# Kernel tuning notes

Measured on AMD Instinct MI355X. Metric: run time of the kernel, lower is better.

## Reference

```python
import jax, jax.numpy as jnp
import numpy as np

IMAGE = 224; P = 16; G = 14; N = 196; C = 3; PD = 768
DIM = 512; DEPTH = 4; H = 8; DH = 64; INNER = 512; MLP = 2048
SCALE = DIM ** -0.5
EPS = 1e-5


def layernorm(x, g, b):
    m = x.mean(-1, keepdims=True)
    v = ((x - m) ** 2).mean(-1, keepdims=True)
    return (x - m) * jax.lax.rsqrt(v + EPS) * g + b


def compute_embedding(W, coords):
    # W: (DIM//2, 2), coords: (b, p, 2) -> (b, p, DIM)
    proj = jnp.einsum('od,bpd->bpo', W, coords)
    s = (2.0 / (DIM // 2)) ** 0.5
    return jnp.concatenate([s * jnp.cos(proj), s * jnp.sin(proj)], axis=-1)


def setup_inputs():
    key = jax.random.key(0)
    ks = jax.random.split(key, 8)
    B = 64
    img = jax.random.normal(ks[0], (B, C, IMAGE, IMAGE), jnp.float32)
    noise_token = jax.random.normal(ks[1], (B, DIM), jnp.float32)
    A_noise = jax.random.normal(ks[2], (B, 2, 2), jnp.float32)
    b_noise = jax.random.normal(ks[3], (B, 2), jnp.float32)
    m, n = np.meshgrid(np.arange(G), np.arange(G))
    X = jnp.asarray(np.reshape(np.stack((m, n), -1), (-1, 2)), jnp.float32)  # (N,2)
    Wfreq = jax.random.normal(ks[4], (DIM // 2, 2), jnp.float32)  # band_width=1.0
    base_pos = compute_embedding(Wfreq, X[None])  # (1,N,DIM), trainable param
    A_mean = jnp.eye(2, dtype=jnp.float32)
    b_mean = jnp.zeros((2,), jnp.float32)
    A_std = jnp.zeros((2, 2), jnp.float32)  # variance_init = 0.0
    b_std = jnp.zeros((2,), jnp.float32)

    def lin(k, i, o):
        return jax.random.normal(k, (i, o), jnp.float32) / np.float32(np.sqrt(i))

    Wpe = lin(ks[5], PD, DIM); bpe = jnp.zeros((DIM,), jnp.float32)
    Wep = lin(ks[6], DIM, PD); bep = jnp.zeros((PD,), jnp.float32)
    kk = jax.random.split(ks[7], DEPTH * 4)
    Wqkv = jnp.stack([lin(kk[4 * i + 0], DIM, 3 * INNER) for i in range(DEPTH)])
    Wout = jnp.stack([lin(kk[4 * i + 1], INNER, DIM) for i in range(DEPTH)])
    bout = jnp.zeros((DEPTH, DIM), jnp.float32)
    Wff1 = jnp.stack([lin(kk[4 * i + 2], DIM, MLP) for i in range(DEPTH)])
    bff1 = jnp.zeros((DEPTH, MLP), jnp.float32)
    Wff2 = jnp.stack([lin(kk[4 * i + 3], MLP, DIM) for i in range(DEPTH)])
    bff2 = jnp.zeros((DEPTH, DIM), jnp.float32)
    ln1_g = jnp.ones((DEPTH, DIM), jnp.float32); ln1_b = jnp.zeros((DEPTH, DIM), jnp.float32)
    ln2_g = jnp.ones((DEPTH, DIM), jnp.float32); ln2_b = jnp.zeros((DEPTH, DIM), jnp.float32)
    return dict(img=img, noise_token=noise_token, A_noise=A_noise, b_noise=b_noise,
                Wfreq=Wfreq, X=X, base_pos=base_pos,
                A_mean=A_mean, b_mean=b_mean, A_std=A_std, b_std=b_std,
                Wpe=Wpe, bpe=bpe, Wep=Wep, bep=bep,
                ln1_g=ln1_g, ln1_b=ln1_b, Wqkv=Wqkv, Wout=Wout, bout=bout,
                ln2_g=ln2_g, ln2_b=ln2_b, Wff1=Wff1, bff1=bff1, Wff2=Wff2, bff2=bff2)


def reference(img, noise_token, A_noise, b_noise, Wfreq, X, base_pos,
              A_mean, b_mean, A_std, b_std, Wpe, bpe, Wep, bep,
              ln1_g, ln1_b, Wqkv, Wout, bout, ln2_g, ln2_b, Wff1, bff1, Wff2, bff2):
    del noise_token  # deleted in original forward
    B = img.shape[0]
    # patchify: b c (h p1) (w p2) -> b (h w) (p1 p2 c)
    x = img.reshape(B, C, G, P, G, P).transpose(0, 2, 4, 3, 5, 1).reshape(B, N, PD)
    x = x @ Wpe + bpe  # patch_to_embedding
    # transformed positional embedding (_compute_transformed_embedding)
    A = A_mean + jax.nn.softplus(A_std) * A_noise          # (B,2,2)
    bvec = b_mean + jax.nn.softplus(b_std) * b_noise       # (B,2)
    X_t = jnp.einsum('pd,bdo->bpo', X, A) + bvec[:, None, :]
    pos = compute_embedding(Wfreq, X_t)                    # (B,N,DIM)
    # pos-only attention scores: identical across layers and heads
    dots = jnp.einsum('bid,jd->bij', pos, base_pos[0]) * SCALE
    attn = jax.nn.softmax(dots, axis=-1)                   # (B,N,N)
    for l in range(DEPTH):
        # PreNorm(SplitAttention) -- note: NO residual around attention
        xn = layernorm(x, ln1_g[l], ln1_b[l])
        qkv = xn @ Wqkv[l]
        v = qkv[..., 2 * INNER:].reshape(B, N, H, DH).transpose(0, 2, 1, 3)  # b h n d
        out = jnp.einsum('bij,bhjd->bhid', attn, v)
        out = out.transpose(0, 2, 1, 3).reshape(B, N, INNER)
        x = out @ Wout[l] + bout[l]
        # Residual(PreNorm(FeedForward))
        xn2 = layernorm(x, ln2_g[l], ln2_b[l])
        ff = jax.nn.gelu(xn2 @ Wff1[l] + bff1[l], approximate=False) @ Wff2[l] + bff2[l]
        x = ff + x
    x = x @ Wep + bep  # embedding_to_patch
    # unpatchify: b (h w) (p1 p2 c) -> b c (h p1) (w p2)
    return x.reshape(B, G, G, P, P, C).transpose(0, 5, 1, 3, 2, 4).reshape(B, C, IMAGE, IMAGE)
```

## Files before the change

### kernel.cpp

```cpp
#include <hip/hip_runtime.h>
#include <hip/hip_bf16.h>
#include <math.h>


#define B_    64
#define NTOK  196
#define CCH   3
#define PDIM  768
#define DIM   512
#define MLP   2048
#define MROWS (B_ * NTOK)
#define IMGHW 224
#define KPAD  224
#define VTLD  (B_ * KPAD)

typedef __attribute__((ext_vector_type(8))) short bf16x8;
typedef __attribute__((ext_vector_type(4))) float f32x4;

static __device__ __forceinline__ unsigned short f2b(float f) {
    unsigned int x = __float_as_uint(f);
    unsigned int r = (x + 0x7FFFu + ((x >> 16) & 1u)) >> 16;
    return (unsigned short)r;
}
static __device__ __forceinline__ float softplusf(float x) {
    return fmaxf(x, 0.0f) + log1pf(expf(-fabsf(x)));
}

typedef const __attribute__((address_space(1))) unsigned int* gp1_t;
typedef __attribute__((address_space(3))) unsigned int* lp3_t;
static __device__ __forceinline__ void gld16(const unsigned short* g, unsigned short* l) {
    __builtin_amdgcn_global_load_lds((gp1_t)g, (lp3_t)l, 16, 0, 0);
}

__global__ __launch_bounds__(256) void patchify_kernel(const float* __restrict__ img,
                                                       unsigned short* __restrict__ xp) {
    long idx = (long)blockIdx.x * blockDim.x + threadIdx.x;
    if (idx >= (long)MROWS * PDIM) return;
    int pd = (int)(idx % PDIM);
    long bn = idx / PDIM;
    int n = (int)(bn % NTOK);
    int b = (int)(bn / NTOK);
    int c = pd % 3;
    int p12 = pd / 3;
    int p1 = p12 >> 4, p2 = p12 & 15;
    int g1 = n / 14, g2 = n % 14;
    long src = (((long)b * CCH + c) * IMGHW + (g1 * 16 + p1)) * IMGHW + (g2 * 16 + p2);
    xp[idx] = f2b(img[src]);
}

__global__ __launch_bounds__(256) void unpatchify_kernel(const float* __restrict__ y,
                                                         float* __restrict__ out) {
    long idx = (long)blockIdx.x * blockDim.x + threadIdx.x;
    if (idx >= (long)B_ * CCH * IMGHW * IMGHW) return;
    int ww = (int)(idx % IMGHW);
    long r = idx / IMGHW;
    int hh = (int)(r % IMGHW);
    r /= IMGHW;
    int c = (int)(r % CCH);
    int b = (int)(r / CCH);
    int g1 = hh >> 4, p1 = hh & 15;
    int g2 = ww >> 4, p2 = ww & 15;
    int n = g1 * 14 + g2;
    int pd = (p1 * 16 + p2) * 3 + c;
    out[idx] = y[((long)b * NTOK + n) * PDIM + pd];
}

__global__ __launch_bounds__(256) void pos_kernel(const float* __restrict__ Xc,
                                                  const float* __restrict__ Wfreq,
                                                  const float* __restrict__ A_noise,
                                                  const float* __restrict__ b_noise,
                                                  const float* __restrict__ A_mean,
                                                  const float* __restrict__ b_mean,
                                                  const float* __restrict__ A_std,
                                                  const float* __restrict__ b_std,
                                                  unsigned short* __restrict__ pos) {
    int bp = blockIdx.x;
    int b = bp / NTOK, p = bp % NTOK;
    int o = threadIdx.x;
    float a00 = A_mean[0] + softplusf(A_std[0]) * A_noise[b * 4 + 0];
    float a01 = A_mean[1] + softplusf(A_std[1]) * A_noise[b * 4 + 1];
    float a10 = A_mean[2] + softplusf(A_std[2]) * A_noise[b * 4 + 2];
    float a11 = A_mean[3] + softplusf(A_std[3]) * A_noise[b * 4 + 3];
    float bv0 = b_mean[0] + softplusf(b_std[0]) * b_noise[b * 2 + 0];
    float bv1 = b_mean[1] + softplusf(b_std[1]) * b_noise[b * 2 + 1];
    float x0 = Xc[p * 2 + 0], x1 = Xc[p * 2 + 1];
    float xt0 = x0 * a00 + x1 * a10 + bv0;
    float xt1 = x0 * a01 + x1 * a11 + bv1;
    float proj = Wfreq[o * 2 + 0] * xt0 + Wfreq[o * 2 + 1] * xt1;
    float sv, cv;
    sincosf(proj, &sv, &cv);
    const float s = 0.08838834764831843f;
    pos[(long)bp * DIM + o]       = f2b(s * cv);
    pos[(long)bp * DIM + 256 + o] = f2b(s * sv);
}

__global__ __launch_bounds__(64) void softmax_kernel(const float* __restrict__ dots,
                                                     unsigned short* __restrict__ attn) {
    long row = blockIdx.x;
    const float* p = dots + row * NTOK;
    unsigned short* q = attn + row * KPAD;
    int t = threadIdx.x;
    float v[4];
    float mx = -INFINITY;
    #pragma unroll
    for (int j = 0; j < 4; j++) {
        int i = t + j * 64;
        v[j] = (i < NTOK) ? p[i] : -INFINITY;
        mx = fmaxf(mx, v[j]);
    }
    #pragma unroll
    for (int off = 32; off >= 1; off >>= 1) mx = fmaxf(mx, __shfl_xor(mx, off));
    float sum = 0.f;
    #pragma unroll
    for (int j = 0; j < 4; j++) {
        int i = t + j * 64;
        v[j] = (i < NTOK) ? expf(v[j] - mx) : 0.f;
        sum += v[j];
    }
    #pragma unroll
    for (int off = 32; off >= 1; off >>= 1) sum += __shfl_xor(sum, off);
    float inv = 1.0f / sum;
    #pragma unroll
    for (int j = 0; j < 4; j++) {
        int i = t + j * 64;
        if (i < NTOK) q[i] = f2b(v[j] * inv);
        else if (i < KPAD) q[i] = 0;
    }
}

__global__ __launch_bounds__(128) void ln_kernel(const float* __restrict__ x,
                                                 const float* __restrict__ g,
                                                 const float* __restrict__ bb,
                                                 unsigned short* __restrict__ out) {
    long row = blockIdx.x;
    int t = threadIdx.x;
    float4 v = *(const float4*)(x + row * DIM + t * 4);
    float s = v.x + v.y + v.z + v.w;
    float q = v.x * v.x + v.y * v.y + v.z * v.z + v.w * v.w;
    #pragma unroll
    for (int off = 32; off >= 1; off >>= 1) {
        s += __shfl_xor(s, off);
        q += __shfl_xor(q, off);
    }
    __shared__ float red[4];
    int lane = t & 63, wv = t >> 6;
    if (lane == 0) { red[wv * 2] = s; red[wv * 2 + 1] = q; }
    __syncthreads();
    float S = red[0] + red[2], Q = red[1] + red[3];
    float mean = S * (1.0f / DIM);
    float var = Q * (1.0f / DIM) - mean * mean;
    float rs = rsqrtf(var + 1e-5f);
    float4 gg = *(const float4*)(g + t * 4);
    float4 bv = *(const float4*)(bb + t * 4);
    ushort4 o;
    o.x = f2b((v.x - mean) * rs * gg.x + bv.x);
    o.y = f2b((v.y - mean) * rs * gg.y + bv.y);
    o.z = f2b((v.z - mean) * rs * gg.z + bv.z);
    o.w = f2b((v.w - mean) * rs * gg.w + bv.w);
    *(ushort4*)(out + row * DIM + t * 4) = o;
}

struct TDesc {
    const float* in;
    unsigned short* out;
    int R, C, ld, cb, bbase, tx, trans;
};
struct TPack { TDesc d[19]; int n; };

__global__ __launch_bounds__(256) void wconv_kernel(TPack p) {
    __shared__ float t[32][33];
    int bid = blockIdx.x;
    int di = 0;
    for (int i = 1; i < p.n; ++i) if (bid >= p.d[i].bbase) di = i;
    TDesc d = p.d[di];
    int local = bid - d.bbase;
    int bx = local % d.tx, by = local / d.tx;
    int r0 = by * 32, c0 = bx * 32;
    int lx = threadIdx.x & 31, ly = threadIdx.x >> 5;
    if (d.trans) {
        #pragma unroll
        for (int i = 0; i < 4; i++) {
            int r = r0 + ly + i * 8, c = c0 + lx;
            t[ly + i * 8][lx] = (r < d.R && c < d.C) ? d.in[(long)r * d.ld + d.cb + c] : 0.f;
        }
        __syncthreads();
        #pragma unroll
        for (int i = 0; i < 4; i++) {
            int c = c0 + ly + i * 8, r = r0 + lx;
            if (c < d.C && r < d.R) d.out[(long)c * d.R + r] = f2b(t[lx][ly + i * 8]);
        }
    } else {
        #pragma unroll
        for (int i = 0; i < 4; i++) {
            int r = r0 + ly + i * 8, c = c0 + lx;
            if (r < d.R && c < d.C) d.out[(long)r * d.C + c] = f2b(d.in[(long)r * d.ld + d.cb + c]);
        }
    }
}

template <bool GELU, bool RESID, bool WF32, bool WB16>
__global__ __launch_bounds__(256) void mgemm(const unsigned short* __restrict__ A,
                                             const unsigned short* __restrict__ Bt,
                                             const float* __restrict__ bias,
                                             const float* __restrict__ Rsd,
                                             float* __restrict__ Cf,
                                             unsigned short* __restrict__ Cb,
                                             int M, int N, int K,
                                             int lda, int ldb, int ldc,
                                             long bsA, long bsBt, long bsC,
                                             float scale, int grp, int gstride) {
    int bz = blockIdx.z;
    A  += bz * bsA;
    Bt += bz * bsBt;
    __shared__ __attribute__((aligned(1024))) unsigned short As[4096];
    __shared__ __attribute__((aligned(1024))) unsigned short Bs[4096];
    int m0 = blockIdx.y * 128, n0 = blockIdx.x * 128;
    int tid = threadIdx.x;
    int wave = tid >> 6, lane = tid & 63;
    int wm = (wave & 1) * 64, wn = (wave >> 1) * 64;
    int fr = lane & 15, fg = lane >> 4;

    int g1 = wave * 64 + lane;
    int g2 = g1 + 256;
    int f1 = g1 >> 7, r1 = g1 & 127;
    int f2 = g2 >> 7, r2 = g2 & 127;
    int ra1 = m0 + r1; if (ra1 > M - 1) ra1 = M - 1;
    int ra2 = m0 + r2; if (ra2 > M - 1) ra2 = M - 1;
    int rb1 = n0 + r1; if (rb1 > N - 1) rb1 = N - 1;
    int rb2 = n0 + r2; if (rb2 > N - 1) rb2 = N - 1;
    const unsigned short* pa1 = A + (long)ra1 * lda + f1 * 8;
    const unsigned short* pa2 = A + (long)ra2 * lda + f2 * 8;
    const unsigned short* pb1 = Bt + (long)rb1 * ldb + f1 * 8;
    const unsigned short* pb2 = Bt + (long)rb2 * ldb + f2 * 8;
    unsigned short* lA1 = &As[wave * 512];
    unsigned short* lA2 = &As[wave * 512 + 2048];
    unsigned short* lB1 = &Bs[wave * 512];
    unsigned short* lB2 = &Bs[wave * 512 + 2048];

    f32x4 acc[4][4];
    #pragma unroll
    for (int i = 0; i < 4; i++)
        #pragma unroll
        for (int j = 0; j < 4; j++) acc[i][j] = (f32x4)0.f;

    for (int k0 = 0; k0 < K; k0 += 32) {
        __syncthreads();
        gld16(pa1 + k0, lA1);
        gld16(pa2 + k0, lA2);
        gld16(pb1 + k0, lB1);
        gld16(pb2 + k0, lB2);
        __syncthreads();
        bf16x8 af[4], bfr[4];
        #pragma unroll
        for (int i = 0; i < 4; i++)
            af[i]  = *(const bf16x8*)&As[(fg * 128 + wm + i * 16 + fr) * 8];
        #pragma unroll
        for (int j = 0; j < 4; j++)
            bfr[j] = *(const bf16x8*)&Bs[(fg * 128 + wn + j * 16 + fr) * 8];
        #pragma unroll
        for (int i = 0; i < 4; i++)
            #pragma unroll
            for (int j = 0; j < 4; j++)
                acc[i][j] = __builtin_amdgcn_mfma_f32_16x16x32_bf16(af[i], bfr[j], acc[i][j], 0, 0, 0);
    }

    long cbase = (long)bz * bsC;
    #pragma unroll
    for (int i = 0; i < 4; i++) {
        int row = m0 + wm + i * 16 + fg * 4;
        #pragma unroll
        for (int j = 0; j < 4; j++) {
            int col = n0 + wn + j * 16 + fr;
            if (col >= N) continue;
            int ocol = (grp > 0) ? ((col / grp) * gstride + (col % grp)) : col;
            float bv = bias ? bias[col] : 0.f;
            #pragma unroll
            for (int r = 0; r < 4; r++) {
                if (row + r >= M) continue;
                float v = acc[i][j][r] * scale + bv;
                if (GELU) v = 0.5f * v * (1.0f + erff(v * 0.70710678118654752f));
                long ci = cbase + (long)(row + r) * ldc + ocol;
                if (RESID) v += Rsd[ci];
                if (WF32) Cf[ci] = v;
                if (WB16) Cb[ci] = f2b(v);
            }
        }
    }
}


extern "C" void kernel_launch(void* const* d_in, const int* in_sizes, int n_in,
                              void* d_out, int out_size, void* d_ws, size_t ws_size,
                              hipStream_t stream) {
    const float* img      = (const float*)d_in[0];
    const float* A_noise  = (const float*)d_in[2];
    const float* b_noise  = (const float*)d_in[3];
    const float* Wfreq    = (const float*)d_in[4];
    const float* Xc       = (const float*)d_in[5];
    const float* base_pos = (const float*)d_in[6];
    const float* A_mean   = (const float*)d_in[7];
    const float* b_mean   = (const float*)d_in[8];
    const float* A_std    = (const float*)d_in[9];
    const float* b_std    = (const float*)d_in[10];
    const float* Wpe      = (const float*)d_in[11];
    const float* bpe      = (const float*)d_in[12];
    const float* Wep      = (const float*)d_in[13];
    const float* bep      = (const float*)d_in[14];
    const float* ln1_g    = (const float*)d_in[15];
    const float* ln1_b    = (const float*)d_in[16];
    const float* Wqkv     = (const float*)d_in[17];
    const float* Wout     = (const float*)d_in[18];
    const float* bout     = (const float*)d_in[19];
    const float* ln2_g    = (const float*)d_in[20];
    const float* ln2_b    = (const float*)d_in[21];
    const float* Wff1     = (const float*)d_in[22];
    const float* bff1     = (const float*)d_in[23];
    const float* Wff2     = (const float*)d_in[24];
    const float* bff2     = (const float*)d_in[25];

    char* ws = (char*)d_ws;
    float*          x_f    = (float*)(ws + 0);
    unsigned short* sb0    = (unsigned short*)(ws + 25690112);
    unsigned short* attn16 = (unsigned short*)(ws + 38535168);
    unsigned short* vT     = (unsigned short*)(ws + 44154880);
    unsigned short* xb16   = (unsigned short*)(ws + 58834944);
    unsigned short* h1     = (unsigned short*)(ws + 71680000);
    unsigned short* pat16  = (unsigned short*)(ws + 71680000);
    unsigned short* pos16  = (unsigned short*)(ws + 90947584);
    float*          dots   = (float*)(ws + 103792640);
    float*          y_f    = (float*)(ws + 71680000);
    char* wp = ws + 123060224;
    unsigned short* WpeT   = (unsigned short*)(wp);
    unsigned short* WqkvT  = (unsigned short*)(wp + 786432);
    unsigned short* WoutT  = (unsigned short*)(wp + 2883584);
    unsigned short* Wff1T  = (unsigned short*)(wp + 4980736);
    unsigned short* Wff2T  = (unsigned short*)(wp + 13369344);
    unsigned short* WepT   = (unsigned short*)(wp + 21757952);
    unsigned short* bp16   = (unsigned short*)(wp + 22544384);

    const float SCALE = 0.044194173824159216f;

    hipMemsetAsync(vT, 0, (size_t)512 * VTLD * 2, stream);

    {
        TPack p; int bb = 0, di = 0;
        auto add = [&](const float* in, unsigned short* out, int R, int C, int ld, int cb, int tr) {
            TDesc d; d.in = in; d.out = out; d.R = R; d.C = C; d.ld = ld; d.cb = cb;
            d.trans = tr; d.tx = (C + 31) / 32; d.bbase = bb;
            bb += d.tx * ((R + 31) / 32);
            p.d[di++] = d;
        };
        add(Wpe, WpeT, 768, 512, 512, 0, 1);
        for (int l = 0; l < 4; l++) add(Wqkv + (long)l * 512 * 1536, WqkvT + (long)l * 512 * 512, 512, 512, 1536, 1024, 1);
        for (int l = 0; l < 4; l++) add(Wout + (long)l * 512 * 512, WoutT + (long)l * 512 * 512, 512, 512, 512, 0, 1);
        for (int l = 0; l < 4; l++) add(Wff1 + (long)l * 512 * 2048, Wff1T + (long)l * 2048 * 512, 512, 2048, 2048, 0, 1);
        for (int l = 0; l < 4; l++) add(Wff2 + (long)l * 2048 * 512, Wff2T + (long)l * 512 * 2048, 2048, 512, 512, 0, 1);
        add(Wep, WepT, 512, 768, 768, 0, 1);
        add(base_pos, bp16, 196, 512, 512, 0, 0);
        p.n = di;
        wconv_kernel<<<dim3(bb), dim3(256), 0, stream>>>(p);
    }

    patchify_kernel<<<dim3((MROWS * PDIM + 255) / 256), dim3(256), 0, stream>>>(img, pat16);
    mgemm<false, false, true, false><<<dim3(4, 98), dim3(256), 0, stream>>>(
        pat16, WpeT, bpe, nullptr, x_f, nullptr, MROWS, DIM, PDIM, PDIM, PDIM, DIM,
        0, 0, 0, 1.0f, 0, 0);
    pos_kernel<<<dim3(MROWS), dim3(256), 0, stream>>>(
        Xc, Wfreq, A_noise, b_noise, A_mean, b_mean, A_std, b_std, pos16);
    mgemm<false, false, true, false><<<dim3(2, 98), dim3(256), 0, stream>>>(
        pos16, bp16, nullptr, nullptr, dots, nullptr, MROWS, NTOK, DIM, DIM, DIM, NTOK,
        0, 0, 0, SCALE, 0, 0);
    softmax_kernel<<<dim3(MROWS), dim3(64), 0, stream>>>(dots, attn16);

    for (int l = 0; l < 4; l++) {
        ln_kernel<<<dim3(MROWS), dim3(128), 0, stream>>>(x_f, ln1_g + l * DIM, ln1_b + l * DIM, sb0);
        mgemm<false, false, false, true><<<dim3(98, 4), dim3(256), 0, stream>>>(
            WqkvT + (long)l * 512 * 512, sb0, nullptr, nullptr, nullptr, vT,
            512, MROWS, DIM, DIM, DIM, VTLD, 0, 0, 0, 1.0f, NTOK, KPAD);
        mgemm<false, false, false, true><<<dim3(4, 2, B_), dim3(256), 0, stream>>>(
            attn16, vT, nullptr, nullptr, nullptr, sb0,
            NTOK, DIM, KPAD, KPAD, VTLD, DIM,
            (long)NTOK * KPAD, (long)KPAD, (long)NTOK * DIM, 1.0f, 0, 0);
        mgemm<false, false, true, false><<<dim3(4, 98), dim3(256), 0, stream>>>(
            sb0, WoutT + (long)l * 512 * 512, bout + l * DIM, nullptr, x_f, nullptr,
            MROWS, DIM, DIM, DIM, DIM, DIM, 0, 0, 0, 1.0f, 0, 0);
        ln_kernel<<<dim3(MROWS), dim3(128), 0, stream>>>(x_f, ln2_g + l * DIM, ln2_b + l * DIM, sb0);
        mgemm<true, false, false, true><<<dim3(16, 98), dim3(256), 0, stream>>>(
            sb0, Wff1T + (long)l * 2048 * 512, bff1 + l * MLP, nullptr, nullptr, h1,
            MROWS, MLP, DIM, DIM, DIM, MLP, 0, 0, 0, 1.0f, 0, 0);
        mgemm<false, true, true, true><<<dim3(4, 98), dim3(256), 0, stream>>>(
            h1, Wff2T + (long)l * 512 * 2048, bff2 + l * DIM, x_f, x_f, xb16,
            MROWS, DIM, MLP, MLP, MLP, DIM, 0, 0, 0, 1.0f, 0, 0);
    }

    mgemm<false, false, true, false><<<dim3(6, 98), dim3(256), 0, stream>>>(
        xb16, WepT, bep, nullptr, y_f, nullptr, MROWS, PDIM, DIM, DIM, DIM, PDIM,
        0, 0, 0, 1.0f, 0, 0);
    unpatchify_kernel<<<dim3(((long)B_ * CCH * IMGHW * IMGHW + 255) / 256), dim3(256), 0, stream>>>(
        y_f, (float*)d_out);
}
```

Baseline: 1.637 ms.

## Double-buffer LDS tiles in mgemm to overlap global loads with MFMA

Doubles the shared-memory A and B tiles to two stages and prefetches the next K-slice with direct global-to-LDS loads while the current slice feeds MFMAs. This cuts one barrier per iteration and is meant to hide global load latency behind compute. It doubles LDS use to 32KB per block, which may lower occupancy. Correctness relies on the async LDS loads being complete at the single barrier before the buffer is read.

```diff
diff --git a/kernel.cpp b/kernel.cpp
--- a/kernel.cpp
+++ b/kernel.cpp
@@ -212,8 +212,8 @@
     int bz = blockIdx.z;
     A  += bz * bsA;
     Bt += bz * bsBt;
-    __shared__ __attribute__((aligned(1024))) unsigned short As[4096];
-    __shared__ __attribute__((aligned(1024))) unsigned short Bs[4096];
+    __shared__ __attribute__((aligned(1024))) unsigned short As[2][4096];
+    __shared__ __attribute__((aligned(1024))) unsigned short Bs[2][4096];
     int m0 = blockIdx.y * 128, n0 = blockIdx.x * 128;
     int tid = threadIdx.x;
     int wave = tid >> 6, lane = tid & 63;
@@ -232,10 +232,8 @@
     const unsigned short* pa2 = A + (long)ra2 * lda + f2 * 8;
     const unsigned short* pb1 = Bt + (long)rb1 * ldb + f1 * 8;
     const unsigned short* pb2 = Bt + (long)rb2 * ldb + f2 * 8;
-    unsigned short* lA1 = &As[wave * 512];
-    unsigned short* lA2 = &As[wave * 512 + 2048];
-    unsigned short* lB1 = &Bs[wave * 512];
-    unsigned short* lB2 = &Bs[wave * 512 + 2048];
+    int lo1 = wave * 512;
+    int lo2 = wave * 512 + 2048;
 
     f32x4 acc[4][4];
     #pragma unroll
@@ -243,25 +241,36 @@
         #pragma unroll
         for (int j = 0; j < 4; j++) acc[i][j] = (f32x4)0.f;
 
-    for (int k0 = 0; k0 < K; k0 += 32) {
-        __syncthreads();
-        gld16(pa1 + k0, lA1);
-        gld16(pa2 + k0, lA2);
-        gld16(pb1 + k0, lB1);
-        gld16(pb2 + k0, lB2);
-        __syncthreads();
+    int nt = K >> 5;
+    gld16(pa1, &As[0][lo1]);
+    gld16(pa2, &As[0][lo2]);
+    gld16(pb1, &Bs[0][lo1]);
+    gld16(pb2, &Bs[0][lo2]);
+    __syncthreads();
+
+    for (int t = 0; t < nt; ++t) {
+        int cur = t & 1;
+        if (t + 1 < nt) {
+            int k0 = (t + 1) << 5;
+            int nxt = cur ^ 1;
+            gld16(pa1 + k0, &As[nxt][lo1]);
+            gld16(pa2 + k0, &As[nxt][lo2]);
+            gld16(pb1 + k0, &Bs[nxt][lo1]);
+            gld16(pb2 + k0, &Bs[nxt][lo2]);
+        }
         bf16x8 af[4], bfr[4];
         #pragma unroll
         for (int i = 0; i < 4; i++)
-            af[i]  = *(const bf16x8*)&As[(fg * 128 + wm + i * 16 + fr) * 8];
+            af[i]  = *(const bf16x8*)&As[cur][(fg * 128 + wm + i * 16 + fr) * 8];
         #pragma unroll
         for (int j = 0; j < 4; j++)
-            bfr[j] = *(const bf16x8*)&Bs[(fg * 128 + wn + j * 16 + fr) * 8];
+            bfr[j] = *(const bf16x8*)&Bs[cur][(fg * 128 + wn + j * 16 + fr) * 8];
         #pragma unroll
         for (int i = 0; i < 4; i++)
             #pragma unroll
             for (int j = 0; j < 4; j++)
                 acc[i][j] = __builtin_amdgcn_mfma_f32_16x16x32_bf16(af[i], bfr[j], acc[i][j], 0, 0, 0);
+        __syncthreads();
     }
 
     long cbase = (long)bz * bsC;
```

After: 1.614 ms. About the same (-1.4%).
